# Kernel optimization log

Hardware: AMD Instinct MI355X
Metric: run time of the kernel (lower is better)

Reference implementation:

```python
import jax, jax.numpy as jnp
import numpy as np

NUM_HEADS = 8
TEMPERATURE = 10000.0


def sine_embed(pos, dim):
    """Sine positional embedding of 2D offsets. pos [..., 2] -> [..., dim]."""
    half = dim // 2  # dims per coordinate
    dim_t = TEMPERATURE ** (2.0 * (jnp.arange(half) // 2).astype(jnp.float32) / half)
    s = pos[..., :, None] / dim_t  # [..., 2, half]
    emb = jnp.stack([jnp.sin(s[..., 0::2]), jnp.cos(s[..., 1::2])], axis=-1)
    emb = emb.reshape(s.shape[:-1] + (half,))  # interleaved sin/cos per coord
    return emb.reshape(pos.shape[:-1] + (dim,))


def setup_inputs() -> dict:
    key = jax.random.key(0)
    ks = jax.random.split(key, 16)
    N, H, W, C, K = 2, 40, 40, 256, 100
    h = NUM_HEADS
    sc = 1.0 / np.sqrt(C)
    return {
        "query_feature": jax.random.normal(ks[0], (N, H, W, C), jnp.float32),
        "query_position": jax.random.uniform(ks[1], (N, H, W, 2), jnp.float32),
        "key_feature": jax.random.normal(ks[2], (N, K, C), jnp.float32),
        "key_position": jax.random.uniform(ks[3], (N, K, 2), jnp.float32),
        # MultiheadAttention params (torch convention: weight [out, in])
        "in_proj_w": jax.random.normal(ks[4], (3 * C, C), jnp.float32) * sc,
        "in_proj_b": jnp.zeros((3 * C,), jnp.float32),
        "out_proj_w": jax.random.normal(ks[5], (C, C), jnp.float32) * sc,
        "out_proj_b": jnp.zeros((C,), jnp.float32),
        # PositionalEncodingSineLearned MLP: sine(C) -> C -> num_heads
        "pos_w1": jax.random.normal(ks[6], (C, C), jnp.float32) * sc,
        "pos_b1": jnp.zeros((C,), jnp.float32),
        "pos_w2": jax.random.normal(ks[7], (h, C), jnp.float32) * sc,
        "pos_b2": jnp.zeros((h,), jnp.float32),
        # cat_pos branch params
        "pos_trans_w": jax.random.normal(ks[8], (2, 2), jnp.float32),
        "embed_w": jax.random.normal(ks[9], (C, C + 2), jnp.float32) * 0.01,
        "embed_b": jnp.zeros((C,), jnp.float32),
    }


def reference(query_feature, query_position, key_feature, key_position,
              in_proj_w, in_proj_b, out_proj_w, out_proj_b,
              pos_w1, pos_b1, pos_w2, pos_b2,
              pos_trans_w, embed_w, embed_b):
    N, H, W, C = query_feature.shape
    h = NUM_HEADS
    d = C // h
    q = query_feature.reshape(N, -1, C)            # [N,Q,C]
    qp = query_position.reshape(N, -1, 2)          # [N,Q,2] (scale_terms = 1.0)
    Q = q.shape[1]
    K = key_feature.shape[1]

    # pairwise relative positions: [N,Q,K,2]
    rel_pos = key_position[:, None, :, :] - qp[:, :, None, :]

    # learned sine relative positional encoding -> per-head additive bias
    pe = sine_embed(rel_pos, C)                              # [N,Q,K,C]
    hid = jax.nn.relu(pe @ pos_w1.T + pos_b1)                # [N,Q,K,C]
    bias = (hid @ pos_w2.T + pos_b2).transpose(0, 3, 1, 2)   # [N,h,Q,K]

    # multihead attention with additive relative bias
    wq, wk, wv = jnp.split(in_proj_w, 3, axis=0)
    bq, bk, bv = jnp.split(in_proj_b, 3, axis=0)
    qh = ((q @ wq.T + bq).reshape(N, Q, h, d)) * (d ** -0.5)
    kh = (key_feature @ wk.T + bk).reshape(N, K, h, d)
    vh = (key_feature @ wv.T + bv).reshape(N, K, h, d)
    scores = jnp.einsum('nqhd,nkhd->nhqk', qh, kh) + bias
    attn = jax.nn.softmax(scores, axis=-1)                   # [N,h,Q,K]
    ctx = jnp.einsum('nhqk,nkhd->nqhd', attn, vh).reshape(N, Q, C)
    refined = ctx @ out_proj_w.T + out_proj_b                # [N,Q,C]

    # cat_pos: attention-weighted relative position aggregation
    attn_w = attn.mean(axis=1)                               # [N,Q,K]
    new_rel = jnp.einsum('nqk,nqkc->nqc', attn_w, jax.lax.stop_gradient(rel_pos))
    new_pos = new_rel @ pos_trans_w.T                        # [N,Q,2]

    feat = jax.nn.relu(q + refined)
    feat = jax.nn.relu(jnp.concatenate([feat, new_pos], axis=-1) @ embed_w.T + embed_b)
    return feat.reshape(N, H, W, C)
```

## Files before the change

kernel.cpp:

```cpp
#include <hip/hip_runtime.h>
#include <math.h>

typedef __bf16 bf16x8 __attribute__((ext_vector_type(8)));
typedef __bf16 bf16x4 __attribute__((ext_vector_type(4)));
typedef float  f32x4  __attribute__((ext_vector_type(4)));


#define WS_KH    0u
#define WS_VH    51200u
#define WS_EWP   102400u
#define WS_QHB   168960u
#define WS_BIASB 578560u
#define WS_KEB   2012160u
#define WS_W1B   2038560u
#define WS_W2PB  2071328u

__device__ __forceinline__ float rdlane(float v, int l) {
  return __uint_as_float(__builtin_amdgcn_readlane(__float_as_uint(v), l));
}

__global__ __launch_bounds__(256, 2) void prep_kernel(
    const float* __restrict__ qfeat, const float* __restrict__ kfeat,
    const float* __restrict__ kpos,
    const float* __restrict__ ipw, const float* __restrict__ ipb,
    const float* __restrict__ pos_w1, const float* __restrict__ pos_w2,
    const float* __restrict__ embed_w, float* __restrict__ ws)
{
  __shared__ float x[8 * 256];
  int bid = blockIdx.x, t = threadIdx.x;

  if (bid < 50) {
    int r = bid * 4 + (t >> 6);
    int u = t & 63;
    float p0 = kpos[r * 2 + 0], p1 = kpos[r * 2 + 1];
    __bf16* keb = (__bf16*)(ws + WS_KEB);
    bf16x4 o;
#pragma unroll
    for (int j = 0; j < 4; j++) {
      int col = u * 4 + j;
      int c = col >> 7, i = (col & 127) >> 1;
      float p = c ? p1 : p0;
      float inv = exp2f((float)i * (-13.287712379549449f / 64.0f));
      float v = p * inv;
      o[j] = (__bf16)((col & 1) ? __cosf(v) : __sinf(v));
    }
    *(bf16x4*)(keb + r * 264 + u * 4) = o;
  } else if (bid < 114) {
    int idx = (bid - 50) * 1024 + t * 4;
    float4 v = *(const float4*)(pos_w1 + idx);
    bf16x4 o; o[0] = (__bf16)v.x; o[1] = (__bf16)v.y; o[2] = (__bf16)v.z; o[3] = (__bf16)v.w;
    *(bf16x4*)((__bf16*)(ws + WS_W1B) + idx) = o;
  } else if (bid == 114) {
    __bf16* w2pb = (__bf16*)(ws + WS_W2PB);
    for (int i = 0; i < 16; i++) {
      int idx = t * 16 + i;
      w2pb[idx] = (idx < 2048) ? (__bf16)pos_w2[idx] : (__bf16)0.0f;
    }
  } else if (bid < 147) {
    int r0 = (bid - 115) * 8;
    for (int rr = 0; rr < 8; rr++) {
      int r = r0 + rr;
      for (int j = t; j < 260; j += 256)
        ws[WS_EWP + r * 260 + j] = (j < 258) ? embed_w[r * 258 + j] : 0.0f;
    }
  } else if (bid < 547) {
    int r0 = (bid - 147) * 8;
    for (int i = t; i < 2048; i += 256) x[i] = qfeat[(unsigned)r0 * 256u + i];
    __syncthreads();
    float acc[8]; float bq = ipb[t];
#pragma unroll
    for (int rr = 0; rr < 8; rr++) acc[rr] = bq;
    const float* wrow = ipw + (unsigned)t * 256u;
    for (int j = 0; j < 256; j += 4) {
      float4 w4 = *(const float4*)(wrow + j);
#pragma unroll
      for (int rr = 0; rr < 8; rr++) {
        float4 x4 = *(const float4*)(x + rr * 256 + j);
        acc[rr] = fmaf(x4.x, w4.x, fmaf(x4.y, w4.y, fmaf(x4.z, w4.z, fmaf(x4.w, w4.w, acc[rr]))));
      }
    }
    __bf16* qhb = (__bf16*)(ws + WS_QHB);
#pragma unroll
    for (int rr = 0; rr < 8; rr++)
      qhb[(unsigned)(r0 + rr) * 256u + t] = (__bf16)(acc[rr] * 0.17677669529663687f);
  } else {
    int b2 = bid - 547; int n = b2 >> 4, tile = b2 & 15;
    int r0l = tile * 7; int cnt = 100 - r0l; if (cnt > 7) cnt = 7; if (cnt <= 0) return;
    int r0 = n * 100 + r0l;
    for (int i = t; i < cnt * 256; i += 256) x[i] = kfeat[(unsigned)r0 * 256u + i];
    __syncthreads();
    float ak[7], av[7]; float bk = ipb[256 + t], bv = ipb[512 + t];
#pragma unroll
    for (int rr = 0; rr < 7; rr++) { ak[rr] = bk; av[rr] = bv; }
    const float* wkr = ipw + (unsigned)(256 + t) * 256u;
    const float* wvr = ipw + (unsigned)(512 + t) * 256u;
    for (int j = 0; j < 256; j += 4) {
      float4 wk4 = *(const float4*)(wkr + j);
      float4 wv4 = *(const float4*)(wvr + j);
#pragma unroll
      for (int rr = 0; rr < 7; rr++) {
        float4 x4 = *(const float4*)(x + rr * 256 + j);
        ak[rr] = fmaf(x4.x, wk4.x, fmaf(x4.y, wk4.y, fmaf(x4.z, wk4.z, fmaf(x4.w, wk4.w, ak[rr]))));
        av[rr] = fmaf(x4.x, wv4.x, fmaf(x4.y, wv4.y, fmaf(x4.z, wv4.z, fmaf(x4.w, wv4.w, av[rr]))));
      }
    }
    for (int rr = 0; rr < 7; rr++) {
      if (rr < cnt) {
        ws[WS_KH + (unsigned)(r0 + rr) * 256u + t] = ak[rr];
        ws[WS_VH + (unsigned)(r0 + rr) * 256u + t] = av[rr];
      }
    }
  }
}

__global__ __launch_bounds__(512) void bias_kernel(
    const float* __restrict__ qpos,
    const float* __restrict__ pos_b1, const float* __restrict__ pos_b2,
    float* __restrict__ ws)
{
  __shared__ __align__(16) char smem[49152];
  __bf16* qe_s = (__bf16*)(smem + 28672);

  int bid = blockIdx.x;
  int n = bid / 200;
  int q0 = bid * 8;
  int t = threadIdx.x;
  int lane = t & 63, w = t >> 6;
  int l15 = lane & 15, quad = lane >> 4;

  const __bf16* keb = (const __bf16*)(ws + WS_KEB) + (unsigned)(n * 100) * 264u;
  const __bf16* w1b = (const __bf16*)(ws + WS_W1B);
  const __bf16* w2pb = (const __bf16*)(ws + WS_W2PB);
  __bf16* biasb = (__bf16*)(ws + WS_BIASB);

  {
    int idx = t * 4;
    int q = idx >> 8, u = idx & 255;
    float p0 = qpos[(q0 + q) * 2 + 0], p1 = qpos[(q0 + q) * 2 + 1];
    bf16x4 o;
#pragma unroll
    for (int j = 0; j < 4; j++) {
      int u2 = u + j;
      int c = u2 >> 7, i = (u2 & 127) >> 1;
      float p = c ? p1 : p0;
      float inv = exp2f((float)i * (-13.287712379549449f / 64.0f));
      float v = p * inv;
      o[j] = (__bf16)((u2 & 1) ? __cosf(v) : __sinf(v));
    }
    *(bf16x4*)(qe_s + idx) = o;
  }

  bf16x8 wfrag[2][8];
#pragma unroll
  for (int ct = 0; ct < 2; ct++)
#pragma unroll
    for (int kc = 0; kc < 8; kc++)
      wfrag[ct][kc] = *(const bf16x8*)(w1b + (unsigned)(w * 32 + ct * 16 + l15) * 256u + kc * 32 + quad * 8);
  float b1v[2][4];
#pragma unroll
  for (int ct = 0; ct < 2; ct++)
#pragma unroll
    for (int r = 0; r < 4; r++) b1v[ct][r] = pos_b1[w * 32 + ct * 16 + quad * 4 + r];
  float b2v[4];
#pragma unroll
  for (int r = 0; r < 4; r++) b2v[r] = pos_b2[(quad * 4 + r) & 7];

  auto gen = [&](int q, int pair, int buf) {
    if (t < 448) {
      int key = t >> 2, sub = t & 3;
      int cb = pair * 64 + sub * 16;
      bf16x8 fr0, fr1;
      const __bf16* qp = qe_s + q * 256 + cb;
      bf16x8 q0f = *(const bf16x8*)qp;
      bf16x8 q1f = *(const bf16x8*)(qp + 8);
      if (key < 100) {
        const __bf16* kp = keb + (unsigned)key * 264u + cb;
        bf16x8 k0f = *(const bf16x8*)kp;
        bf16x8 k1f = *(const bf16x8*)(kp + 8);
#pragma unroll
        for (int jj = 0; jj < 4; jj++) {
          float sk = (float)k0f[2 * jj], ck = (float)k0f[2 * jj + 1];
          float sq = (float)q0f[2 * jj], cq = (float)q0f[2 * jj + 1];
          fr0[2 * jj]     = (__bf16)(sk * cq - ck * sq);
          fr0[2 * jj + 1] = (__bf16)(ck * cq + sk * sq);
          float sk1 = (float)k1f[2 * jj], ck1 = (float)k1f[2 * jj + 1];
          float sq1 = (float)q1f[2 * jj], cq1 = (float)q1f[2 * jj + 1];
          fr1[2 * jj]     = (__bf16)(sk1 * cq1 - ck1 * sq1);
          fr1[2 * jj + 1] = (__bf16)(ck1 * cq1 + sk1 * sq1);
        }
      } else {
#pragma unroll
        for (int jj = 0; jj < 8; jj++) { fr0[jj] = (__bf16)0.f; fr1[jj] = (__bf16)0.f; }
      }
      int mt = key >> 4, kl = key & 15;
      int kcl = sub >> 1;
      int qd0 = (sub & 1) * 2;
      bf16x8* dst = (bf16x8*)smem + buf * 896 + kcl * 448 + mt * 64 + qd0 * 16 + kl;
      dst[0] = fr0;
      dst[16] = fr1;
    }
  };

  f32x4 zero4; zero4[0] = 0.f; zero4[1] = 0.f; zero4[2] = 0.f; zero4[3] = 0.f;

  __syncthreads();
  gen(0, 0, 0);
  __syncthreads();

  for (int q = 0; q < 8; q++) {
    f32x4 acc[2][7];
#pragma unroll
    for (int ct = 0; ct < 2; ct++)
#pragma unroll
      for (int mt = 0; mt < 7; mt++) acc[ct][mt] = zero4;

    for (int p = 0; p < 4; p++) {
      if (p < 3) gen(q, p + 1, (p + 1) & 1);
      else if (q < 7) gen(q + 1, 0, 0);
      const bf16x8* pb = (const bf16x8*)smem + (p & 1) * 896;
#pragma unroll
      for (int kh = 0; kh < 2; kh++) {
        int kc = p * 2 + kh;
        bf16x8 pf[7];
#pragma unroll
        for (int mt = 0; mt < 7; mt++) pf[mt] = pb[kh * 448 + mt * 64 + lane];
#pragma unroll
        for (int mt = 0; mt < 7; mt++) {
          acc[0][mt] = __builtin_amdgcn_mfma_f32_16x16x32_bf16(wfrag[0][kc], pf[mt], acc[0][mt], 0, 0, 0);
          acc[1][mt] = __builtin_amdgcn_mfma_f32_16x16x32_bf16(wfrag[1][kc], pf[mt], acc[1][mt], 0, 0, 0);
        }
      }
      __syncthreads();
    }

#pragma unroll
    for (int ct = 0; ct < 2; ct++)
#pragma unroll
      for (int mt = 0; mt < 7; mt++)
#pragma unroll
        for (int r = 0; r < 4; r++)
          acc[ct][mt][r] = fmaxf(acc[ct][mt][r] + b1v[ct][r], 0.0f);

    __bf16* region = (__bf16*)(smem + 32768);
    auto wreg = [&](int mt, int rb) {
#pragma unroll
      for (int ct = 0; ct < 2; ct++) {
        int qt = ct * 2 + (quad >> 1);
        int j0 = (quad & 1) * 4;
        bf16x4 o;
#pragma unroll
        for (int r = 0; r < 4; r++) o[r] = (__bf16)acc[ct][mt][r];
        *(bf16x4*)(region + rb * 4096 + ((w * 64 + qt * 16 + l15) << 3) + j0) = o;
      }
    };
    wreg(0, 0);
    __syncthreads();
    for (int mt = 0; mt < 7; mt++) {
      if (w == mt) {
        f32x4 acc2 = zero4;
        const bf16x8* rg = (const bf16x8*)region + (mt & 1) * 512;
#pragma unroll
        for (int s = 0; s < 8; s++) {
          bf16x8 w2f = *(const bf16x8*)(w2pb + (unsigned)l15 * 256u + s * 32 + quad * 8);
          bf16x8 hf = rg[s * 64 + lane];
          acc2 = __builtin_amdgcn_mfma_f32_16x16x32_bf16(w2f, hf, acc2, 0, 0, 0);
        }
        if (quad < 2) {
          bf16x4 o;
#pragma unroll
          for (int r = 0; r < 4; r++) o[r] = (__bf16)(acc2[r] + b2v[r]);
          *(bf16x4*)(biasb + ((unsigned)(q0 + q) * 112u + mt * 16 + l15) * 8u + quad * 4) = o;
        }
      }
      if (mt < 6) wreg(mt + 1, (mt + 1) & 1);
      __syncthreads();
    }
  }
}

__global__ __launch_bounds__(256, 4) void attn_kernel(
    const float* __restrict__ qfeat, const float* __restrict__ qpos,
    const float* __restrict__ kpos,
    const float* __restrict__ out_w, const float* __restrict__ out_b,
    const float* __restrict__ embed_b, const float* __restrict__ ptw,
    const float* __restrict__ ws, float* __restrict__ out)
{
  __shared__ float qh_s[4 * 8 * 36];
  __shared__ float attn_s[4 * 8 * 116];
  __shared__ float ctx_s[4 * 264];
  __shared__ float cat_s[4 * 264];
  __shared__ float aw_s[4 * 104];

  int bid = blockIdx.x;
  int qg0 = bid * 4;
  int n = bid / 400;
  int t = threadIdx.x;

  const __bf16* qhb = (const __bf16*)(ws + WS_QHB);
  const __bf16* biasb = (const __bf16*)(ws + WS_BIASB);
  const float* kh = ws + WS_KH;
  const float* vh = ws + WS_VH;
  const float* ewp = ws + WS_EWP;

  for (int i = t; i < 1024; i += 256) {
    int q = i >> 8, c = i & 255;
    qh_s[(q * 8 + (c >> 5)) * 36 + (c & 31)] = (float)qhb[(unsigned)(qg0 + q) * 256u + c];
  }
  __syncthreads();

  for (int i = 0; i < 4; i++) {
    int p = t + i * 256;
    if (p < 800) {
      int k = p >> 3, h = p & 7;
      const float4* kf = (const float4*)(kh + (unsigned)(n * 100 + k) * 256u + h * 32);
      float4 kv[8];
#pragma unroll
      for (int dd = 0; dd < 8; dd++) kv[dd] = kf[dd];
#pragma unroll
      for (int q = 0; q < 4; q++) {
        const float4* qf = (const float4*)(qh_s + (q * 8 + h) * 36);
        float s = (float)biasb[((unsigned)(qg0 + q) * 112u + k) * 8u + h];
#pragma unroll
        for (int dd = 0; dd < 8; dd++) {
          float4 qv = qf[dd];
          s += kv[dd].x * qv.x + kv[dd].y * qv.y + kv[dd].z * qv.z + kv[dd].w * qv.w;
        }
        attn_s[(q * 8 + h) * 116 + k] = s;
      }
    }
  }
  __syncthreads();

  {
    int q = t >> 6, h = (t >> 3) & 7, j = t & 7;
    float* row = attn_s + (q * 8 + h) * 116;
    float mx = -1e30f;
    for (int k = j; k < 100; k += 8) mx = fmaxf(mx, row[k]);
    mx = fmaxf(mx, __shfl_xor(mx, 1, 8));
    mx = fmaxf(mx, __shfl_xor(mx, 2, 8));
    mx = fmaxf(mx, __shfl_xor(mx, 4, 8));
    float sum = 0.f;
    for (int k = j; k < 100; k += 8) { float e = __expf(row[k] - mx); row[k] = e; sum += e; }
    sum += __shfl_xor(sum, 1, 8);
    sum += __shfl_xor(sum, 2, 8);
    sum += __shfl_xor(sum, 4, 8);
    float inv = 1.0f / sum;
    for (int k = j; k < 100; k += 8) row[k] *= inv;
  }
  __syncthreads();

  for (int p = t; p < 416; p += 256) {
    int q = p / 104, k = p % 104;
    if (k < 100) {
      float s = 0.f;
#pragma unroll
      for (int h = 0; h < 8; h++) s += attn_s[(q * 8 + h) * 116 + k];
      aw_s[q * 104 + k] = s * 0.125f;
    }
  }
  {
    int c = t, h = c >> 5;
    float a0 = 0.f, a1 = 0.f, a2 = 0.f, a3 = 0.f;
    const float* vp = vh + (unsigned)(n * 100) * 256u + c;
    const float* r0 = attn_s + (0 * 8 + h) * 116;
    const float* r1 = attn_s + (1 * 8 + h) * 116;
    const float* r2 = attn_s + (2 * 8 + h) * 116;
    const float* r3 = attn_s + (3 * 8 + h) * 116;
#pragma unroll 4
    for (int k = 0; k < 100; k++) {
      float vv = vp[(unsigned)k * 256u];
      a0 = fmaf(r0[k], vv, a0);
      a1 = fmaf(r1[k], vv, a1);
      a2 = fmaf(r2[k], vv, a2);
      a3 = fmaf(r3[k], vv, a3);
    }
    ctx_s[0 * 264 + c] = a0; ctx_s[1 * 264 + c] = a1;
    ctx_s[2 * 264 + c] = a2; ctx_s[3 * 264 + c] = a3;
  }
  __syncthreads();

  if (t < 8) {
    int q = t >> 1, cd = t & 1;
    float qp = qpos[(qg0 + q) * 2 + cd];
    float s = 0.f;
    for (int k = 0; k < 100; k++)
      s = fmaf(aw_s[q * 104 + k], kpos[(n * 100 + k) * 2 + cd] - qp, s);
    float so = __shfl_xor(s, 1, 2);
    if (cd == 0) cat_s[q * 264 + 256] = ptw[0] * s + ptw[1] * so;
    else         cat_s[q * 264 + 257] = ptw[2] * so + ptw[3] * s;
  }

  {
    int c = t, lane = t & 63;
    float ob = out_b[c];
    float acc0 = ob, acc1 = ob, acc2 = ob, acc3 = ob;
    const float* wr = out_w + (unsigned)c * 256u;
    for (int ch = 0; ch < 4; ch++) {
      float v0 = ctx_s[0 * 264 + ch * 64 + lane];
      float v1 = ctx_s[1 * 264 + ch * 64 + lane];
      float v2 = ctx_s[2 * 264 + ch * 64 + lane];
      float v3 = ctx_s[3 * 264 + ch * 64 + lane];
      const float* wp = wr + ch * 64;
#pragma unroll 4
      for (int j4 = 0; j4 < 16; j4++) {
        float4 w4 = *(const float4*)(wp + j4 * 4);
        int jb = j4 * 4;
        acc0 = fmaf(rdlane(v0, jb + 0), w4.x, acc0);
        acc1 = fmaf(rdlane(v1, jb + 0), w4.x, acc1);
        acc2 = fmaf(rdlane(v2, jb + 0), w4.x, acc2);
        acc3 = fmaf(rdlane(v3, jb + 0), w4.x, acc3);
        acc0 = fmaf(rdlane(v0, jb + 1), w4.y, acc0);
        acc1 = fmaf(rdlane(v1, jb + 1), w4.y, acc1);
        acc2 = fmaf(rdlane(v2, jb + 1), w4.y, acc2);
        acc3 = fmaf(rdlane(v3, jb + 1), w4.y, acc3);
        acc0 = fmaf(rdlane(v0, jb + 2), w4.z, acc0);
        acc1 = fmaf(rdlane(v1, jb + 2), w4.z, acc1);
        acc2 = fmaf(rdlane(v2, jb + 2), w4.z, acc2);
        acc3 = fmaf(rdlane(v3, jb + 2), w4.z, acc3);
        acc0 = fmaf(rdlane(v0, jb + 3), w4.w, acc0);
        acc1 = fmaf(rdlane(v1, jb + 3), w4.w, acc1);
        acc2 = fmaf(rdlane(v2, jb + 3), w4.w, acc2);
        acc3 = fmaf(rdlane(v3, jb + 3), w4.w, acc3);
      }
    }
    cat_s[0 * 264 + c] = fmaxf(qfeat[(unsigned)(qg0 + 0) * 256u + c] + acc0, 0.f);
    cat_s[1 * 264 + c] = fmaxf(qfeat[(unsigned)(qg0 + 1) * 256u + c] + acc1, 0.f);
    cat_s[2 * 264 + c] = fmaxf(qfeat[(unsigned)(qg0 + 2) * 256u + c] + acc2, 0.f);
    cat_s[3 * 264 + c] = fmaxf(qfeat[(unsigned)(qg0 + 3) * 256u + c] + acc3, 0.f);
  }
  __syncthreads();

  {
    int c = t, lane = t & 63;
    float eb = embed_b[c];
    float acc0 = eb, acc1 = eb, acc2 = eb, acc3 = eb;
    const float* er = ewp + (unsigned)c * 260u;
    for (int ch = 0; ch < 4; ch++) {
      float v0 = cat_s[0 * 264 + ch * 64 + lane];
      float v1 = cat_s[1 * 264 + ch * 64 + lane];
      float v2 = cat_s[2 * 264 + ch * 64 + lane];
      float v3 = cat_s[3 * 264 + ch * 64 + lane];
      const float* wp = er + ch * 64;
#pragma unroll 4
      for (int j4 = 0; j4 < 16; j4++) {
        float4 w4 = *(const float4*)(wp + j4 * 4);
        int jb = j4 * 4;
        acc0 = fmaf(rdlane(v0, jb + 0), w4.x, acc0);
        acc1 = fmaf(rdlane(v1, jb + 0), w4.x, acc1);
        acc2 = fmaf(rdlane(v2, jb + 0), w4.x, acc2);
        acc3 = fmaf(rdlane(v3, jb + 0), w4.x, acc3);
        acc0 = fmaf(rdlane(v0, jb + 1), w4.y, acc0);
        acc1 = fmaf(rdlane(v1, jb + 1), w4.y, acc1);
        acc2 = fmaf(rdlane(v2, jb + 1), w4.y, acc2);
        acc3 = fmaf(rdlane(v3, jb + 1), w4.y, acc3);
        acc0 = fmaf(rdlane(v0, jb + 2), w4.z, acc0);
        acc1 = fmaf(rdlane(v1, jb + 2), w4.z, acc1);
        acc2 = fmaf(rdlane(v2, jb + 2), w4.z, acc2);
        acc3 = fmaf(rdlane(v3, jb + 2), w4.z, acc3);
        acc0 = fmaf(rdlane(v0, jb + 3), w4.w, acc0);
        acc1 = fmaf(rdlane(v1, jb + 3), w4.w, acc1);
        acc2 = fmaf(rdlane(v2, jb + 3), w4.w, acc2);
        acc3 = fmaf(rdlane(v3, jb + 3), w4.w, acc3);
      }
    }
    float4 wt = *(const float4*)(er + 256);
    acc0 += cat_s[0 * 264 + 256] * wt.x + cat_s[0 * 264 + 257] * wt.y;
    acc1 += cat_s[1 * 264 + 256] * wt.x + cat_s[1 * 264 + 257] * wt.y;
    acc2 += cat_s[2 * 264 + 256] * wt.x + cat_s[2 * 264 + 257] * wt.y;
    acc3 += cat_s[3 * 264 + 256] * wt.x + cat_s[3 * 264 + 257] * wt.y;
    out[(unsigned)(qg0 + 0) * 256u + c] = fmaxf(acc0, 0.f);
    out[(unsigned)(qg0 + 1) * 256u + c] = fmaxf(acc1, 0.f);
    out[(unsigned)(qg0 + 2) * 256u + c] = fmaxf(acc2, 0.f);
    out[(unsigned)(qg0 + 3) * 256u + c] = fmaxf(acc3, 0.f);
  }
}

extern "C" void kernel_launch(void* const* d_in, const int* in_sizes, int n_in,
                              void* d_out, int out_size, void* d_ws, size_t ws_size,
                              hipStream_t stream)
{
  const float* query_feature  = (const float*)d_in[0];
  const float* query_position = (const float*)d_in[1];
  const float* key_feature    = (const float*)d_in[2];
  const float* key_position   = (const float*)d_in[3];
  const float* in_proj_w      = (const float*)d_in[4];
  const float* in_proj_b      = (const float*)d_in[5];
  const float* out_proj_w     = (const float*)d_in[6];
  const float* out_proj_b     = (const float*)d_in[7];
  const float* pos_w1         = (const float*)d_in[8];
  const float* pos_b1         = (const float*)d_in[9];
  const float* pos_w2         = (const float*)d_in[10];
  const float* pos_b2         = (const float*)d_in[11];
  const float* pos_trans_w    = (const float*)d_in[12];
  const float* embed_w        = (const float*)d_in[13];
  const float* embed_b        = (const float*)d_in[14];
  float* ws  = (float*)d_ws;
  float* out = (float*)d_out;

  hipLaunchKernelGGL(prep_kernel, dim3(579), dim3(256), 0, stream,
                     query_feature, key_feature, key_position,
                     in_proj_w, in_proj_b, pos_w1, pos_w2, embed_w, ws);
  hipLaunchKernelGGL(bias_kernel, dim3(400), dim3(512), 0, stream,
                     query_position, pos_b1, pos_b2, ws);
  hipLaunchKernelGGL(attn_kernel, dim3(800), dim3(256), 0, stream,
                     query_feature, query_position, key_position,
                     out_proj_w, out_proj_b, embed_b, pos_trans_w,
                     ws, out);
}
```

Baseline: 301.3 us.

## Split bias kernel into smaller blocks, swizzle LDS, parallelize second projection

The bias kernel now processes 4 queries per block instead of 8, doubling the grid to 800 blocks so more CUs stay busy. The shared-memory fragment layout gains an XOR swizzle on writes and reads, aimed at cutting LDS bank conflicts. The second (hidden-to-heads) projection now writes four hidden tiles at once and runs its MFMA on four waves in parallel, in two phases, instead of one wave per tile with a barrier after each. In exchange each block uses more LDS, which may lower occupancy, and fixed per-block setup such as loading the weight fragments is repeated across twice as many blocks.

```diff
diff --git a/kernel.cpp b/kernel.cpp
--- a/kernel.cpp
+++ b/kernel.cpp
@@ -118,12 +118,13 @@
     const float* __restrict__ pos_b1, const float* __restrict__ pos_b2,
     float* __restrict__ ws)
 {
-  __shared__ __align__(16) char smem[49152];
-  __bf16* qe_s = (__bf16*)(smem + 28672);
+  __shared__ __align__(16) char smem[63488];
+  __bf16* qe_s   = (__bf16*)(smem + 28672);
+  __bf16* region = (__bf16*)(smem + 30720);
 
   int bid = blockIdx.x;
-  int n = bid / 200;
-  int q0 = bid * 8;
+  int n = bid / 400;
+  int q0 = bid * 4;
   int t = threadIdx.x;
   int lane = t & 63, w = t >> 6;
   int l15 = lane & 15, quad = lane >> 4;
@@ -134,20 +135,14 @@
   __bf16* biasb = (__bf16*)(ws + WS_BIASB);
 
   {
-    int idx = t * 4;
+    int idx = t * 2;
     int q = idx >> 8, u = idx & 255;
-    float p0 = qpos[(q0 + q) * 2 + 0], p1 = qpos[(q0 + q) * 2 + 1];
-    bf16x4 o;
-#pragma unroll
-    for (int j = 0; j < 4; j++) {
-      int u2 = u + j;
-      int c = u2 >> 7, i = (u2 & 127) >> 1;
-      float p = c ? p1 : p0;
-      float inv = exp2f((float)i * (-13.287712379549449f / 64.0f));
-      float v = p * inv;
-      o[j] = (__bf16)((u2 & 1) ? __cosf(v) : __sinf(v));
-    }
-    *(bf16x4*)(qe_s + idx) = o;
+    int c = u >> 7, i = (u & 127) >> 1;
+    float p = qpos[(q0 + q) * 2 + c];
+    float inv = exp2f((float)i * (-13.287712379549449f / 64.0f));
+    float v = p * inv;
+    qe_s[idx]     = (__bf16)__sinf(v);
+    qe_s[idx + 1] = (__bf16)__cosf(v);
   }
 
   bf16x8 wfrag[2][8];
@@ -195,9 +190,9 @@
       int mt = key >> 4, kl = key & 15;
       int kcl = sub >> 1;
       int qd0 = (sub & 1) * 2;
-      bf16x8* dst = (bf16x8*)smem + buf * 896 + kcl * 448 + mt * 64 + qd0 * 16 + kl;
-      dst[0] = fr0;
-      dst[16] = fr1;
+      bf16x8* base = (bf16x8*)smem + buf * 896 + kcl * 448 + mt * 64;
+      base[qd0 * 16 + (kl ^ (qd0 * 2 + kcl))]             = fr0;
+      base[(qd0 + 1) * 16 + (kl ^ (qd0 * 2 + 2 + kcl))]   = fr1;
     }
   };
 
@@ -207,7 +202,7 @@
   gen(0, 0, 0);
   __syncthreads();
 
-  for (int q = 0; q < 8; q++) {
+  for (int q = 0; q < 4; q++) {
     f32x4 acc[2][7];
 #pragma unroll
     for (int ct = 0; ct < 2; ct++)
@@ -216,14 +211,15 @@
 
     for (int p = 0; p < 4; p++) {
       if (p < 3) gen(q, p + 1, (p + 1) & 1);
-      else if (q < 7) gen(q + 1, 0, 0);
+      else if (q < 3) gen(q + 1, 0, 0);
       const bf16x8* pb = (const bf16x8*)smem + (p & 1) * 896;
 #pragma unroll
       for (int kh = 0; kh < 2; kh++) {
         int kc = p * 2 + kh;
         bf16x8 pf[7];
 #pragma unroll
-        for (int mt = 0; mt < 7; mt++) pf[mt] = pb[kh * 448 + mt * 64 + lane];
+        for (int mt = 0; mt < 7; mt++)
+          pf[mt] = pb[kh * 448 + mt * 64 + quad * 16 + (l15 ^ (quad * 2 + kh))];
 #pragma unroll
         for (int mt = 0; mt < 7; mt++) {
           acc[0][mt] = __builtin_amdgcn_mfma_f32_16x16x32_bf16(wfrag[0][kc], pf[mt], acc[0][mt], 0, 0, 0);
@@ -241,8 +237,7 @@
         for (int r = 0; r < 4; r++)
           acc[ct][mt][r] = fmaxf(acc[ct][mt][r] + b1v[ct][r], 0.0f);
 
-    __bf16* region = (__bf16*)(smem + 32768);
-    auto wreg = [&](int mt, int rb) {
+    auto wreg = [&](int mt, int slot) {
 #pragma unroll
       for (int ct = 0; ct < 2; ct++) {
         int qt = ct * 2 + (quad >> 1);
@@ -250,31 +245,33 @@
         bf16x4 o;
 #pragma unroll
         for (int r = 0; r < 4; r++) o[r] = (__bf16)acc[ct][mt][r];
-        *(bf16x4*)(region + rb * 4096 + ((w * 64 + qt * 16 + l15) << 3) + j0) = o;
+        *(bf16x4*)(region + slot * 4096 + ((w * 64 + qt * 16 + l15) << 3) + j0) = o;
       }
     };
-    wreg(0, 0);
+    auto g2 = [&](int mt, int slot) {
+      f32x4 acc2 = zero4;
+      const bf16x8* rg = (const bf16x8*)(region + slot * 4096);
+#pragma unroll
+      for (int s = 0; s < 8; s++) {
+        bf16x8 w2f = *(const bf16x8*)(w2pb + (unsigned)l15 * 256u + s * 32 + quad * 8);
+        bf16x8 hf = rg[s * 64 + lane];
+        acc2 = __builtin_amdgcn_mfma_f32_16x16x32_bf16(w2f, hf, acc2, 0, 0, 0);
+      }
+      if (quad < 2) {
+        bf16x4 o;
+#pragma unroll
+        for (int r = 0; r < 4; r++) o[r] = (__bf16)(acc2[r] + b2v[r]);
+        *(bf16x4*)(biasb + ((unsigned)(q0 + q) * 112u + mt * 16 + l15) * 8u + quad * 4) = o;
+      }
+    };
+
+    wreg(0, 0); wreg(1, 1); wreg(2, 2); wreg(3, 3);
     __syncthreads();
-    for (int mt = 0; mt < 7; mt++) {
-      if (w == mt) {
-        f32x4 acc2 = zero4;
-        const bf16x8* rg = (const bf16x8*)region + (mt & 1) * 512;
-#pragma unroll
-        for (int s = 0; s < 8; s++) {
-          bf16x8 w2f = *(const bf16x8*)(w2pb + (unsigned)l15 * 256u + s * 32 + quad * 8);
-          bf16x8 hf = rg[s * 64 + lane];
-          acc2 = __builtin_amdgcn_mfma_f32_16x16x32_bf16(w2f, hf, acc2, 0, 0, 0);
-        }
-        if (quad < 2) {
-          bf16x4 o;
-#pragma unroll
-          for (int r = 0; r < 4; r++) o[r] = (__bf16)(acc2[r] + b2v[r]);
-          *(bf16x4*)(biasb + ((unsigned)(q0 + q) * 112u + mt * 16 + l15) * 8u + quad * 4) = o;
-        }
-      }
-      if (mt < 6) wreg(mt + 1, (mt + 1) & 1);
-      __syncthreads();
-    }
+    if (w < 4) g2(w, w);
+    __syncthreads();
+    wreg(4, 0); wreg(5, 1); wreg(6, 2);
+    __syncthreads();
+    if (w < 3) g2(4 + w, w);
   }
 }
 
@@ -500,7 +497,7 @@
   hipLaunchKernelGGL(prep_kernel, dim3(579), dim3(256), 0, stream,
                      query_feature, key_feature, key_position,
                      in_proj_w, in_proj_b, pos_w1, pos_w2, embed_w, ws);
-  hipLaunchKernelGGL(bias_kernel, dim3(400), dim3(512), 0, stream,
+  hipLaunchKernelGGL(bias_kernel, dim3(800), dim3(512), 0, stream,
                      query_position, pos_b1, pos_b2, ws);
   hipLaunchKernelGGL(attn_kernel, dim3(800), dim3(256), 0, stream,
                      query_feature, query_position, key_position,
```

After: 295.1 us. -2.1%, faster.
